# Optimization experiments

Measured on AMD Instinct MI355X. Metric: run time of the kernel, lower is better.

The kernel has to match this reference:

```python
import math
import jax, jax.numpy as jnp
import numpy as np

N, M = 2048, 128            # fine grid points, coarse points
IN_NF, H, LMAX = 256, 128, 2
A2B = 1.88973
MIN_STD = 0.32 * A2B / 2.0  # two stddevs reach min covalent radius (Bohr)
MAX_STD = 2.32 * A2B / 2.0


def _sph_lmax2(d):
    # norm-normalized real spherical harmonics (e3nn convention), unit input d[..., 3]
    x, y, z = d[..., 0], d[..., 1], d[..., 2]
    s3 = math.sqrt(3.0)
    sh0 = jnp.ones_like(x)[..., None]                                    # [., 1]
    sh1 = jnp.stack([x, y, z], axis=-1)                                  # [., 3]
    sh2 = jnp.stack([s3 * x * z, s3 * x * y,
                     y * y - 0.5 * (x * x + z * z),
                     s3 * y * z, 0.5 * s3 * (z * z - x * x)], axis=-1)   # [., 5]
    return [sh0, sh1, sh2]


def _radial(dist, nb):
    # Gaussian radial basis; two stddevs span [MIN_COV_RAD, MAX_COV_RAD]
    s = jnp.linspace(MIN_STD, MAX_STD, nb, dtype=dist.dtype)
    temps = 2.0 * s * s
    x2 = dist[..., None] ** 2
    return jnp.exp(-x2 / temps) * (2.0 / 3.0) * x2 / temps / (math.pi * temps) ** 1.5


def setup_inputs():
    key = jax.random.key(0)
    k = jax.random.split(key, 10)
    xav = math.sqrt(6.0 / (H + H))
    return {
        'h': jax.random.normal(k[0], (N, IN_NF), jnp.float32),
        'grid_coords': jax.random.normal(k[1], (N, 3), jnp.float32),
        'coarse_coords': jax.random.normal(k[2], (M, 3), jnp.float32),
        'grid_weights': jax.random.uniform(k[3], (N,), jnp.float32),
        'W_pre': jax.random.normal(k[4], (IN_NF, H), jnp.float32) * math.sqrt(2.0 / (IN_NF + H)),
        'b_pre': jnp.zeros((H,), jnp.float32),
        'W_down': jax.random.uniform(k[5], (LMAX + 1, H, H), jnp.float32, -xav, xav),
        'W_up': jax.random.uniform(k[6], (LMAX + 1, H, H), jnp.float32, -xav, xav),
        'W_post': jax.random.normal(k[7], (H, H), jnp.float32) * math.sqrt(2.0 / (H + H)),
        'b_post': jnp.zeros((H,), jnp.float32),
    }


def reference(h, grid_coords, coarse_coords, grid_weights,
              W_pre, b_pre, W_down, W_up, W_post, b_post):
    h = jax.nn.silu(h @ W_pre + b_pre)                            # [N, H]
    # all-pairs directions/distances (vect_cdist); radius_cutoff = inf -> every pair is an edge
    dvec = grid_coords[:, None, :] - coarse_coords[None, :, :]    # [N, M, 3]
    dist = jnp.sqrt((dvec * dvec + 1e-20).sum(-1))                # [N, M]
    dirs = dvec / dist[..., None]
    sh = _sph_lmax2(dirs)                                         # list of [N, M, 2l+1]
    rad = _radial(dist, H)                                        # [N, M, H]
    # tp_down: paths (0e x le -> le); l=0 uses the scalar branch (no 1/sqrt(2l+1))
    # radial gating per hidden channel + quadrature integration onto coarse nodes
    coarse = []
    for l in range(LMAX + 1):
        norm = 1.0 if l == 0 else math.sqrt(2 * l + 1)
        c = jnp.einsum('nu,uw,nmj,nmw,n->mwj',
                       h, W_down[l], sh[l], rad, grid_weights) / norm
        coarse.append(c)                                          # [M, H, 2l+1]
    # tp_up: paths (le x le -> 0e); l>0 branch divides by sqrt(2l+1); scatter back to grid
    out = 0.0
    for l in range(LMAX + 1):
        norm = 1.0 if l == 0 else math.sqrt(2 * l + 1)
        out = out + jnp.einsum('mui,uw,nmi->nw', coarse[l], W_up[l], sh[l]) / norm
    return jax.nn.silu(out @ W_post + b_post)                     # [N, H]
```

## Files before the change

kernel.cpp:

```cpp
#include <hip/hip_runtime.h>
#include <math.h>

#define N_PTS 2048
#define M_PTS 128
#define INNF  256
#define H     128

#define MIN_STDC 0.30235680f
#define MAX_STDC 2.19208680f
#define PI_F     3.14159265358979f
#define LOG2E_F  1.44269504089f

static __device__ __forceinline__ float silu_f(float x) {
  return x / (1.0f + __expf(-x));
}

__global__ __launch_bounds__(256) void k_pre(const float* __restrict__ h,
    const float* __restrict__ W_pre, const float* __restrict__ b_pre,
    const float* __restrict__ W_down, const float* __restrict__ gw,
    float* __restrict__ hdg4) {
  __shared__ float bigW[12288];
  __shared__ float h_t[8 * INNF];
  __shared__ float hp_t[8 * H];
  int t = threadIdx.x;
  int n0 = blockIdx.x * 8;
  int lw = t & 31;
  int g  = t >> 5;
  int w0 = lw * 4;

  #pragma unroll
  for (int i = 0; i < 2; ++i) {
    int idx = t + i * 256;
    int row = idx >> 6, col = (idx & 63) << 2;
    *(float4*)&h_t[row * INNF + col] =
        *(const float4*)(h + (size_t)(n0 + row) * INNF + col);
  }

  float acc[4] = {};
  for (int kc = 0; kc < 256; kc += 64) {
    __syncthreads();
    #pragma unroll
    for (int i = 0; i < 8; ++i) {
      int idx = t + i * 256;
      *(float4*)&bigW[idx * 4] = *(const float4*)(W_pre + (size_t)kc * H + idx * 4);
    }
    __syncthreads();
    #pragma unroll 4
    for (int u4 = 0; u4 < 16; ++u4) {
      float4 hv = *(const float4*)&h_t[g * INNF + kc + u4 * 4];
      float hvv[4] = {hv.x, hv.y, hv.z, hv.w};
      #pragma unroll
      for (int uu = 0; uu < 4; ++uu) {
        float4 wv = *(const float4*)&bigW[(u4 * 4 + uu) * H + w0];
        acc[0] += hvv[uu] * wv.x; acc[1] += hvv[uu] * wv.y;
        acc[2] += hvv[uu] * wv.z; acc[3] += hvv[uu] * wv.w;
      }
    }
  }
  {
    float4 bv = *(const float4*)(b_pre + w0);
    float4 o = make_float4(silu_f(acc[0] + bv.x), silu_f(acc[1] + bv.y),
                           silu_f(acc[2] + bv.z), silu_f(acc[3] + bv.w));
    __syncthreads();
    *(float4*)&hp_t[g * H + w0] = o;
  }

  float acc2[3][4] = {};
  for (int kc = 0; kc < 128; kc += 32) {
    __syncthreads();
    #pragma unroll
    for (int i = 0; i < 12; ++i) {
      int idx = t + i * 256;
      int l = idx >> 10, r4 = idx & 1023;
      *(float4*)&bigW[idx * 4] =
          *(const float4*)(W_down + ((size_t)l * H + kc) * H + r4 * 4);
    }
    __syncthreads();
    #pragma unroll 2
    for (int u4 = 0; u4 < 8; ++u4) {
      float4 pv = *(const float4*)&hp_t[g * H + kc + u4 * 4];
      float pvv[4] = {pv.x, pv.y, pv.z, pv.w};
      #pragma unroll
      for (int uu = 0; uu < 4; ++uu) {
        int ul = u4 * 4 + uu;
        #pragma unroll
        for (int l = 0; l < 3; ++l) {
          float4 wv = *(const float4*)&bigW[(l * 32 + ul) * H + w0];
          acc2[l][0] += pvv[uu] * wv.x; acc2[l][1] += pvv[uu] * wv.y;
          acc2[l][2] += pvv[uu] * wv.z; acc2[l][3] += pvv[uu] * wv.w;
        }
      }
    }
  }

  {
    const float stp = (MAX_STDC - MIN_STDC) / 127.0f;
    const float invn1 = 0.57735026919f, invn2 = 0.44721359550f;
    int n = n0 + g;
    float gwv = gw[n];
    #pragma unroll
    for (int i = 0; i < 4; ++i) {
      int w = w0 + i;
      float s = MIN_STDC + (float)w * stp;
      float temps = 2.0f * s * s;
      float coef = (2.0f / 3.0f) / (temps * powf(PI_F * temps, 1.5f));
      float sc = gwv * coef;
      *(float4*)(hdg4 + ((size_t)n * H + w) * 4) =
          make_float4(acc2[0][i] * sc, acc2[1][i] * sc * invn1,
                      acc2[2][i] * sc * invn2, 0.0f);
    }
  }
}

__global__ __launch_bounds__(256, 4) void k_down(const float* __restrict__ gc,
    const float* __restrict__ cc, const float* __restrict__ hdg4,
    float* __restrict__ c_part) {
  __shared__ float lds[9216];
  int t = threadIdx.x;
  int m0 = blockIdx.x * 4;
  int ss = blockIdx.y;
  int n0 = ss * 64;
  int wv = t >> 6;
  int ln = t & 63;
  int w0 = ln * 2;

  {
    int n_loc = t >> 2, m_loc = t & 3;
    int n = n0 + n_loc, m = m0 + m_loc;
    float dx = gc[3*n]   - cc[3*m];
    float dy = gc[3*n+1] - cc[3*m+1];
    float dz = gc[3*n+2] - cc[3*m+2];
    float d2 = dx*dx + dy*dy + dz*dz + 3e-20f;
    float inv = rsqrtf(d2);
    float x = dx*inv, y = dy*inv, z = dz*inv;
    const float s3 = 1.73205080757f;
    float* dst = &lds[(size_t)t * 12];
    *(float4*)(dst)     = make_float4(1.0f, x, y, z);
    *(float4*)(dst + 4) = make_float4(s3*x*z, s3*x*y,
                                      y*y - 0.5f*(x*x + z*z), s3*y*z);
    *(float4*)(dst + 8) = make_float4(0.5f*s3*(z*z - x*x), d2, 0.0f, 0.0f);
  }
  __syncthreads();

  const float stp = (MAX_STDC - MIN_STDC) / 127.0f;
  float sA = MIN_STDC + (float)w0 * stp;
  float sB = MIN_STDC + (float)(w0 + 1) * stp;
  float cA = -LOG2E_F / (2.0f * sA * sA);
  float cB = -LOG2E_F / (2.0f * sB * sB);

  float acc[4][9][2] = {};
  for (int j = 0; j < 16; ++j) {
    int nl = wv * 16 + j;
    const float4* hb = (const float4*)(hdg4 + ((size_t)(n0 + nl) * H + w0) * 4);
    float4 hv0 = hb[0];
    float4 hv1 = hb[1];
    const float* shb = &lds[(size_t)nl * 48];
    #pragma unroll
    for (int mm = 0; mm < 4; ++mm) {
      float4 q0 = *(const float4*)(shb + mm*12);
      float4 q1 = *(const float4*)(shb + mm*12 + 4);
      float4 q2 = *(const float4*)(shb + mm*12 + 8);
      float e0 = exp2f(q2.y * cA);
      float e1 = exp2f(q2.y * cB);
      float rp0 = e0 * q2.y, rp1 = e1 * q2.y;
      float a00 = hv0.x*rp0, a01 = hv0.y*rp0, a02 = hv0.z*rp0;
      float a10 = hv1.x*rp1, a11 = hv1.y*rp1, a12 = hv1.z*rp1;
      acc[mm][0][0] += a00;        acc[mm][0][1] += a10;
      acc[mm][1][0] += a01*q0.y;   acc[mm][1][1] += a11*q0.y;
      acc[mm][2][0] += a01*q0.z;   acc[mm][2][1] += a11*q0.z;
      acc[mm][3][0] += a01*q0.w;   acc[mm][3][1] += a11*q0.w;
      acc[mm][4][0] += a02*q1.x;   acc[mm][4][1] += a12*q1.x;
      acc[mm][5][0] += a02*q1.y;   acc[mm][5][1] += a12*q1.y;
      acc[mm][6][0] += a02*q1.z;   acc[mm][6][1] += a12*q1.z;
      acc[mm][7][0] += a02*q1.w;   acc[mm][7][1] += a12*q1.w;
      acc[mm][8][0] += a02*q2.x;   acc[mm][8][1] += a12*q2.x;
    }
  }

  __syncthreads();
  if (wv & 1) {
    float* dst = &lds[(wv >> 1) * 4608];
    #pragma unroll
    for (int mm = 0; mm < 4; ++mm)
      #pragma unroll
      for (int li = 0; li < 9; ++li)
        *(float2*)&dst[(mm*9 + li)*128 + w0] =
            make_float2(acc[mm][li][0], acc[mm][li][1]);
  }
  __syncthreads();
  if (!(wv & 1)) {
    const float* src = &lds[(wv >> 1) * 4608];
    #pragma unroll
    for (int mm = 0; mm < 4; ++mm)
      #pragma unroll
      for (int li = 0; li < 9; ++li) {
        float2 v = *(const float2*)&src[(mm*9 + li)*128 + w0];
        acc[mm][li][0] += v.x; acc[mm][li][1] += v.y;
      }
  }
  __syncthreads();
  if (wv == 2) {
    #pragma unroll
    for (int mm = 0; mm < 4; ++mm)
      #pragma unroll
      for (int li = 0; li < 9; ++li)
        *(float2*)&lds[(mm*9 + li)*128 + w0] =
            make_float2(acc[mm][li][0], acc[mm][li][1]);
  }
  __syncthreads();
  if (wv == 0) {
    #pragma unroll
    for (int mm = 0; mm < 4; ++mm)
      #pragma unroll
      for (int li = 0; li < 9; ++li) {
        float2 v = *(const float2*)&lds[(mm*9 + li)*128 + w0];
        float2 o = make_float2(acc[mm][li][0] + v.x, acc[mm][li][1] + v.y);
        *(float2*)&c_part[(((size_t)ss*M_PTS + m0 + mm)*9 + li)*H + w0] = o;
      }
  }
}

__global__ __launch_bounds__(128) void k_cu(const float* __restrict__ c_part,
    const float* __restrict__ W_up, float* __restrict__ CU9) {
  __shared__ float c_lds[H];
  int t = threadIdx.x;
  int m = blockIdx.x, li = blockIdx.y;
  float v = 0.0f;
  #pragma unroll
  for (int s = 0; s < 32; ++s)
    v += c_part[(((size_t)s*M_PTS + m)*9 + li)*H + t];
  c_lds[t] = v;
  __syncthreads();

  int l = (li == 0) ? 0 : (li < 4 ? 1 : 2);
  const float invn[3] = {1.0f, 0.57735026919f, 0.44721359550f};
  float acc = 0.0f;
  for (int u = 0; u < H; u += 4) {
    float w0 = W_up[((size_t)l*H + u + 0)*H + t];
    float w1 = W_up[((size_t)l*H + u + 1)*H + t];
    float w2 = W_up[((size_t)l*H + u + 2)*H + t];
    float w3 = W_up[((size_t)l*H + u + 3)*H + t];
    acc += c_lds[u]*w0 + c_lds[u+1]*w1 + c_lds[u+2]*w2 + c_lds[u+3]*w3;
  }
  CU9[((size_t)m*9 + li)*H + t] = acc * invn[l];
}

__global__ __launch_bounds__(256) void k_up(const float* __restrict__ gc,
    const float* __restrict__ cc, const float* __restrict__ CU9,
    float* __restrict__ out_part) {
  __shared__ float At[72 * 36];
  __shared__ float Bl[72 * 128];
  int t = threadIdx.x;
  int n0 = blockIdx.x * 32;
  int ks = blockIdx.y;
  int wq  = t & 31;
  int tgn = t >> 5;
  int w0 = wq * 4;
  float acc[4][4] = {};

  for (int ch = 0; ch < 2; ++ch) {
    int m0 = ks*16 + ch*8;
    if (ch) __syncthreads();
    {
      int n_loc = t >> 3, mrel = t & 7;
      int n = n0 + n_loc, m = m0 + mrel;
      float dx = gc[3*n]   - cc[3*m];
      float dy = gc[3*n+1] - cc[3*m+1];
      float dz = gc[3*n+2] - cc[3*m+2];
      float d2 = dx*dx + dy*dy + dz*dz + 3e-20f;
      float inv = rsqrtf(d2);
      float x = dx*inv, y = dy*inv, z = dz*inv;
      const float s3 = 1.73205080757f;
      float sh[9];
      sh[0] = 1.0f; sh[1] = x; sh[2] = y; sh[3] = z;
      sh[4] = s3*x*z; sh[5] = s3*x*y; sh[6] = y*y - 0.5f*(x*x + z*z);
      sh[7] = s3*y*z; sh[8] = 0.5f*s3*(z*z - x*x);
      #pragma unroll
      for (int li = 0; li < 9; ++li)
        At[(mrel*9 + li)*36 + n_loc] = sh[li];
    }
    #pragma unroll
    for (int i = 0; i < 9; ++i) {
      int idx = t + i*256;
      *(float4*)&Bl[idx*4] = *(const float4*)(CU9 + (size_t)m0*9*H + idx*4);
    }
    __syncthreads();

    #pragma unroll 8
    for (int k = 0; k < 72; ++k) {
      float4 a = *(const float4*)&At[k*36 + 4*tgn];
      float4 b = *(const float4*)&Bl[k*128 + w0];
      float av[4] = {a.x, a.y, a.z, a.w};
      float bv[4] = {b.x, b.y, b.z, b.w};
      #pragma unroll
      for (int r = 0; r < 4; ++r)
        #pragma unroll
        for (int c = 0; c < 4; ++c)
          acc[r][c] += av[r] * bv[c];
    }
  }
  #pragma unroll
  for (int r = 0; r < 4; ++r) {
    size_t row = (size_t)ks*N_PTS + n0 + 4*tgn + r;
    *(float4*)(out_part + row*H + w0) =
        make_float4(acc[r][0], acc[r][1], acc[r][2], acc[r][3]);
  }
}

__global__ __launch_bounds__(256) void k_post(const float* __restrict__ out_part,
    const float* __restrict__ W_post, const float* __restrict__ b_post,
    float* __restrict__ out) {
  __shared__ float op[4 * H];
  int t = threadIdx.x;
  int n0 = blockIdx.x * 4;
  int w = t & 127, nh = t >> 7;

  #pragma unroll
  for (int i = 0; i < 2; ++i) {
    int idx = t + i*256;
    int nl = idx >> 7, ww = idx & 127;
    float v = 0.0f;
    #pragma unroll
    for (int s = 0; s < 8; ++s)
      v += out_part[((size_t)s*N_PTS + n0 + nl)*H + ww];
    op[nl*H + ww] = v;
  }
  __syncthreads();

  float acc[2] = {0.0f, 0.0f};
  for (int u = 0; u < H; u += 4) {
    float4 p0 = *(const float4*)&op[(nh*2 + 0)*H + u];
    float4 p1 = *(const float4*)&op[(nh*2 + 1)*H + u];
    float w0 = W_post[(u+0)*H + w];
    float w1 = W_post[(u+1)*H + w];
    float w2 = W_post[(u+2)*H + w];
    float w3 = W_post[(u+3)*H + w];
    acc[0] += p0.x*w0 + p0.y*w1 + p0.z*w2 + p0.w*w3;
    acc[1] += p1.x*w0 + p1.y*w1 + p1.z*w2 + p1.w*w3;
  }
  float bp = b_post[w];
  out[(size_t)(n0 + nh*2 + 0)*H + w] = silu_f(acc[0] + bp);
  out[(size_t)(n0 + nh*2 + 1)*H + w] = silu_f(acc[1] + bp);
}

extern "C" void kernel_launch(void* const* d_in, const int* in_sizes, int n_in,
                              void* d_out, int out_size, void* d_ws, size_t ws_size,
                              hipStream_t stream) {
  const float* h      = (const float*)d_in[0];
  const float* gc     = (const float*)d_in[1];
  const float* cc     = (const float*)d_in[2];
  const float* gw     = (const float*)d_in[3];
  const float* W_pre  = (const float*)d_in[4];
  const float* b_pre  = (const float*)d_in[5];
  const float* W_down = (const float*)d_in[6];
  const float* W_up   = (const float*)d_in[7];
  const float* W_post = (const float*)d_in[8];
  const float* b_post = (const float*)d_in[9];

  float* ws       = (float*)d_ws;
  float* hdg4     = ws;
  float* c_part   = hdg4 + 1048576;
  float* CU9      = c_part + 4718592;
  float* out_part = c_part;
  float* out      = (float*)d_out;

  k_pre <<<256,           256, 0, stream>>>(h, W_pre, b_pre, W_down, gw, hdg4);
  k_down<<<dim3(32,32),   256, 0, stream>>>(gc, cc, hdg4, c_part);
  k_cu  <<<dim3(128,9),   128, 0, stream>>>(c_part, W_up, CU9);
  k_up  <<<dim3(64,8),    256, 0, stream>>>(gc, cc, CU9, out_part);
  k_post<<<512,           256, 0, stream>>>(out_part, W_post, b_post, out);
}
```

Measured before the change: 143.1 us.

## Enlarge k_down grid tiles and fuse harmonic computation into k_up register tiles

k_down now processes 128 grid points per block instead of 64, halving the number of partial coarse sums written and reduced in k_cu. k_up is restructured to load all 16 coarse points' CU9 rows into LDS once and compute spherical harmonics directly in registers for 8 grid rows per thread, removing the transposed At staging buffer and one synchronisation round. This trades fewer blocks and redundant per-thread rsqrt/harmonic work, plus larger LDS use, for less memory traffic and fewer barriers.

Measured after the change: 149.6 us. 1.05x slower.

```diff
diff --git a/kernel.cpp b/kernel.cpp
--- a/kernel.cpp
+++ b/kernel.cpp
@@ -119,13 +119,15 @@
   int t = threadIdx.x;
   int m0 = blockIdx.x * 4;
   int ss = blockIdx.y;
-  int n0 = ss * 64;
+  int n0 = ss * 128;
   int wv = t >> 6;
   int ln = t & 63;
   int w0 = ln * 2;
 
-  {
-    int n_loc = t >> 2, m_loc = t & 3;
+  #pragma unroll
+  for (int i = 0; i < 2; ++i) {
+    int idx = t + i * 256;
+    int n_loc = idx >> 2, m_loc = idx & 3;
     int n = n0 + n_loc, m = m0 + m_loc;
     float dx = gc[3*n]   - cc[3*m];
     float dy = gc[3*n+1] - cc[3*m+1];
@@ -134,7 +136,7 @@
     float inv = rsqrtf(d2);
     float x = dx*inv, y = dy*inv, z = dz*inv;
     const float s3 = 1.73205080757f;
-    float* dst = &lds[(size_t)t * 12];
+    float* dst = &lds[(size_t)idx * 12];
     *(float4*)(dst)     = make_float4(1.0f, x, y, z);
     *(float4*)(dst + 4) = make_float4(s3*x*z, s3*x*y,
                                       y*y - 0.5f*(x*x + z*z), s3*y*z);
@@ -149,8 +151,8 @@
   float cB = -LOG2E_F / (2.0f * sB * sB);
 
   float acc[4][9][2] = {};
-  for (int j = 0; j < 16; ++j) {
-    int nl = wv * 16 + j;
+  for (int j = 0; j < 32; ++j) {
+    int nl = wv * 32 + j;
     const float4* hb = (const float4*)(hdg4 + ((size_t)(n0 + nl) * H + w0) * 4);
     float4 hv0 = hb[0];
     float4 hv1 = hb[1];
@@ -227,7 +229,7 @@
   int m = blockIdx.x, li = blockIdx.y;
   float v = 0.0f;
   #pragma unroll
-  for (int s = 0; s < 32; ++s)
+  for (int s = 0; s < 16; ++s)
     v += c_part[(((size_t)s*M_PTS + m)*9 + li)*H + t];
   c_lds[t] = v;
   __syncthreads();
@@ -248,60 +250,74 @@
 __global__ __launch_bounds__(256) void k_up(const float* __restrict__ gc,
     const float* __restrict__ cc, const float* __restrict__ CU9,
     float* __restrict__ out_part) {
-  __shared__ float At[72 * 36];
-  __shared__ float Bl[72 * 128];
-  int t = threadIdx.x;
-  int n0 = blockIdx.x * 32;
+  __shared__ float Bl[16 * 9 * 128];
+  int t = threadIdx.x;
+  int n0 = blockIdx.x * 64;
   int ks = blockIdx.y;
-  int wq  = t & 31;
-  int tgn = t >> 5;
+  int wq = t & 31;
+  int ng = t >> 5;
   int w0 = wq * 4;
-  float acc[4][4] = {};
-
-  for (int ch = 0; ch < 2; ++ch) {
-    int m0 = ks*16 + ch*8;
-    if (ch) __syncthreads();
-    {
-      int n_loc = t >> 3, mrel = t & 7;
-      int n = n0 + n_loc, m = m0 + mrel;
-      float dx = gc[3*n]   - cc[3*m];
-      float dy = gc[3*n+1] - cc[3*m+1];
-      float dz = gc[3*n+2] - cc[3*m+2];
+
+  #pragma unroll
+  for (int i = 0; i < 18; ++i) {
+    int idx = t + i * 256;
+    *(float4*)&Bl[idx * 4] =
+        *(const float4*)(CU9 + (size_t)(ks * 16) * 9 * H + idx * 4);
+  }
+
+  float gx[8], gy[8], gz[8];
+  #pragma unroll
+  for (int r = 0; r < 8; ++r) {
+    int n = n0 + ng * 8 + r;
+    gx[r] = gc[3*n]; gy[r] = gc[3*n+1]; gz[r] = gc[3*n+2];
+  }
+  __syncthreads();
+
+  float acc[8][4] = {};
+  for (int mr = 0; mr < 16; ++mr) {
+    int m = ks * 16 + mr;
+    float cx = cc[3*m], cy = cc[3*m+1], cz = cc[3*m+2];
+    float4 B0 = *(const float4*)&Bl[(mr*9 + 0)*128 + w0];
+    float4 B1 = *(const float4*)&Bl[(mr*9 + 1)*128 + w0];
+    float4 B2 = *(const float4*)&Bl[(mr*9 + 2)*128 + w0];
+    float4 B3 = *(const float4*)&Bl[(mr*9 + 3)*128 + w0];
+    float4 B4 = *(const float4*)&Bl[(mr*9 + 4)*128 + w0];
+    float4 B5 = *(const float4*)&Bl[(mr*9 + 5)*128 + w0];
+    float4 B6 = *(const float4*)&Bl[(mr*9 + 6)*128 + w0];
+    float4 B7 = *(const float4*)&Bl[(mr*9 + 7)*128 + w0];
+    float4 B8 = *(const float4*)&Bl[(mr*9 + 8)*128 + w0];
+    #pragma unroll
+    for (int r = 0; r < 8; ++r) {
+      float dx = gx[r]-cx, dy = gy[r]-cy, dz = gz[r]-cz;
       float d2 = dx*dx + dy*dy + dz*dz + 3e-20f;
       float inv = rsqrtf(d2);
       float x = dx*inv, y = dy*inv, z = dz*inv;
       const float s3 = 1.73205080757f;
-      float sh[9];
-      sh[0] = 1.0f; sh[1] = x; sh[2] = y; sh[3] = z;
-      sh[4] = s3*x*z; sh[5] = s3*x*y; sh[6] = y*y - 0.5f*(x*x + z*z);
-      sh[7] = s3*y*z; sh[8] = 0.5f*s3*(z*z - x*x);
-      #pragma unroll
-      for (int li = 0; li < 9; ++li)
-        At[(mrel*9 + li)*36 + n_loc] = sh[li];
-    }
-    #pragma unroll
-    for (int i = 0; i < 9; ++i) {
-      int idx = t + i*256;
-      *(float4*)&Bl[idx*4] = *(const float4*)(CU9 + (size_t)m0*9*H + idx*4);
-    }
-    __syncthreads();
-
-    #pragma unroll 8
-    for (int k = 0; k < 72; ++k) {
-      float4 a = *(const float4*)&At[k*36 + 4*tgn];
-      float4 b = *(const float4*)&Bl[k*128 + w0];
-      float av[4] = {a.x, a.y, a.z, a.w};
-      float bv[4] = {b.x, b.y, b.z, b.w};
-      #pragma unroll
-      for (int r = 0; r < 4; ++r)
-        #pragma unroll
-        for (int c = 0; c < 4; ++c)
-          acc[r][c] += av[r] * bv[c];
-    }
-  }
-  #pragma unroll
-  for (int r = 0; r < 4; ++r) {
-    size_t row = (size_t)ks*N_PTS + n0 + 4*tgn + r;
+      float s4 = s3*x*z, s5 = s3*x*y, s6 = y*y - 0.5f*(x*x + z*z);
+      float s7 = s3*y*z, s8 = 0.5f*s3*(z*z - x*x);
+      acc[r][0] += B0.x;        acc[r][1] += B0.y;
+      acc[r][2] += B0.z;        acc[r][3] += B0.w;
+      acc[r][0] += x*B1.x;      acc[r][1] += x*B1.y;
+      acc[r][2] += x*B1.z;      acc[r][3] += x*B1.w;
+      acc[r][0] += y*B2.x;      acc[r][1] += y*B2.y;
+      acc[r][2] += y*B2.z;      acc[r][3] += y*B2.w;
+      acc[r][0] += z*B3.x;      acc[r][1] += z*B3.y;
+      acc[r][2] += z*B3.z;      acc[r][3] += z*B3.w;
+      acc[r][0] += s4*B4.x;     acc[r][1] += s4*B4.y;
+      acc[r][2] += s4*B4.z;     acc[r][3] += s4*B4.w;
+      acc[r][0] += s5*B5.x;     acc[r][1] += s5*B5.y;
+      acc[r][2] += s5*B5.z;     acc[r][3] += s5*B5.w;
+      acc[r][0] += s6*B6.x;     acc[r][1] += s6*B6.y;
+      acc[r][2] += s6*B6.z;     acc[r][3] += s6*B6.w;
+      acc[r][0] += s7*B7.x;     acc[r][1] += s7*B7.y;
+      acc[r][2] += s7*B7.z;     acc[r][3] += s7*B7.w;
+      acc[r][0] += s8*B8.x;     acc[r][1] += s8*B8.y;
+      acc[r][2] += s8*B8.z;     acc[r][3] += s8*B8.w;
+    }
+  }
+  #pragma unroll
+  for (int r = 0; r < 8; ++r) {
+    size_t row = (size_t)ks*N_PTS + n0 + ng*8 + r;
     *(float4*)(out_part + row*H + w0) =
         make_float4(acc[r][0], acc[r][1], acc[r][2], acc[r][3]);
   }
@@ -360,13 +376,13 @@
   float* ws       = (float*)d_ws;
   float* hdg4     = ws;
   float* c_part   = hdg4 + 1048576;
-  float* CU9      = c_part + 4718592;
+  float* CU9      = c_part + 2359296;
   float* out_part = c_part;
   float* out      = (float*)d_out;
 
   k_pre <<<256,           256, 0, stream>>>(h, W_pre, b_pre, W_down, gw, hdg4);
-  k_down<<<dim3(32,32),   256, 0, stream>>>(gc, cc, hdg4, c_part);
+  k_down<<<dim3(32,16),   256, 0, stream>>>(gc, cc, hdg4, c_part);
   k_cu  <<<dim3(128,9),   128, 0, stream>>>(c_part, W_up, CU9);
-  k_up  <<<dim3(64,8),    256, 0, stream>>>(gc, cc, CU9, out_part);
+  k_up  <<<dim3(32,8),    256, 0, stream>>>(gc, cc, CU9, out_part);
   k_post<<<512,           256, 0, stream>>>(out_part, W_post, b_post, out);
 }
```
